# Performance work log

Measured on AMD Instinct MI355X. Metric: run time of the kernel, lower is better.

Reference implementation:

```python
import jax, jax.numpy as jnp
import numpy as np
from math import sqrt

B, N, M, HID, NH = 16, 512, 1024, 512, 8
HS = HID // NH  # 64


def layer_norm(x, g, b, eps=1e-5):
    mu = jnp.mean(x, axis=-1, keepdims=True)
    var = jnp.var(x, axis=-1, keepdims=True)
    return (x - mu) * jax.lax.rsqrt(var + eps) * g + b


def apply_moverz(x, s, c):
    # x: [B, L, NH, HS]; s, c: [B, L, 1, HS//2]
    x0, x1 = x[..., 0::2], x[..., 1::2]
    return jnp.concatenate([x0 * c - x1 * s, x1 * c + x0 * s], axis=-1)


def attention(q, k, v, mask):
    # q: [B,Nq,NH,HS], k/v: [B,Nk,NH,HS], mask broadcastable to [B,NH,Nq,Nk]
    attn = jnp.einsum('bnhd,bmhd->bhnm', q, k) / sqrt(HS)
    attn = jnp.where(mask, -jnp.inf, attn)
    attn = jax.nn.softmax(attn, axis=-1)
    x = jnp.einsum('bhnm,bmhd->bnhd', attn, v)
    return x.reshape(x.shape[0], x.shape[1], HID)


def setup_inputs() -> dict:
    key = jax.random.key(0)
    ks = jax.random.split(key, 24)
    inp = {}
    inp['tgt'] = jax.random.normal(ks[0], (B, N, HID), dtype=jnp.float32)
    inp['mem'] = jax.random.normal(ks[1], (B, M, HID), dtype=jnp.float32)
    th_p = jax.random.uniform(ks[2], (B, N, 1, HS // 2), dtype=jnp.float32) * (2 * np.pi)
    th_k = jax.random.uniform(ks[3], (B, M, 1, HS // 2), dtype=jnp.float32) * (2 * np.pi)
    inp['pep_mass_sin'] = jnp.sin(th_p)
    inp['pep_mass_cos'] = jnp.cos(th_p)
    inp['peaks_moverz_sin'] = jnp.sin(th_k)
    inp['peaks_moverz_cos'] = jnp.cos(th_k)
    # causal self-attn mask (True = masked)
    inp['tgt_mask'] = jnp.triu(jnp.ones((N, N), dtype=bool), k=1)[None, None]
    # pad last 64 memory positions
    pad = jnp.arange(M) >= (M - 64)
    inp['mem_key_padding_mask'] = jnp.broadcast_to(pad[None, None, None, :], (B, 1, 1, M))
    s = 0.02
    w = lambda i, shape: jax.random.normal(ks[i], shape, dtype=jnp.float32) * s
    # MaskedMultiHeadAttn params
    inp['mmha_w'] = w(4, (3 * HID, HID)); inp['mmha_b'] = jnp.zeros((3 * HID,), jnp.float32)
    inp['mmha_ow'] = w(5, (HID, HID)); inp['mmha_ob'] = jnp.zeros((HID,), jnp.float32)
    inp['mmha_g'] = jnp.ones((HID,), jnp.float32); inp['mmha_beta'] = jnp.zeros((HID,), jnp.float32)
    # MultiHeadAttn (cross) params
    inp['mha_qw'] = w(6, (HID, HID)); inp['mha_qb'] = jnp.zeros((HID,), jnp.float32)
    inp['mha_kvw'] = w(7, (2 * HID, HID)); inp['mha_kvb'] = jnp.zeros((2 * HID,), jnp.float32)
    inp['mha_ow'] = w(8, (HID, HID)); inp['mha_ob'] = jnp.zeros((HID,), jnp.float32)
    inp['mha_g'] = jnp.ones((HID,), jnp.float32); inp['mha_beta'] = jnp.zeros((HID,), jnp.float32)
    # FFN params (no bias)
    inp['ffn_w1'] = w(9, (4 * HID, HID))
    inp['ffn_w2'] = w(10, (HID, 4 * HID))
    inp['ffn_g'] = jnp.ones((HID,), jnp.float32); inp['ffn_beta'] = jnp.zeros((HID,), jnp.float32)
    return inp


def reference(tgt, mem, pep_mass_sin, pep_mass_cos, peaks_moverz_sin, peaks_moverz_cos,
              tgt_mask, mem_key_padding_mask,
              mmha_w, mmha_b, mmha_ow, mmha_ob, mmha_g, mmha_beta,
              mha_qw, mha_qb, mha_kvw, mha_kvb, mha_ow, mha_ob, mha_g, mha_beta,
              ffn_w1, ffn_w2, ffn_g, ffn_beta):
    # --- masked self-attention ---
    qkv = (tgt @ mmha_w.T + mmha_b).reshape(B, N, NH, 3 * HS)
    q, k, v = jnp.split(qkv, 3, axis=-1)
    x = attention(q, k, v, tgt_mask)
    tgt = layer_norm(x @ mmha_ow.T + mmha_ob + tgt, mmha_g, mmha_beta)
    # --- cross-attention with moverz distance bias ---
    q = (tgt @ mha_qw.T + mha_qb).reshape(B, N, NH, HS)
    q = apply_moverz(q, pep_mass_sin, pep_mass_cos)
    kv = (mem @ mha_kvw.T + mha_kvb).reshape(B, M, NH, 2 * HS)
    k, v = jnp.split(kv, 2, axis=-1)
    k = apply_moverz(k, peaks_moverz_sin, peaks_moverz_cos)
    x = attention(q, k, v, mem_key_padding_mask)
    tgt = layer_norm(x @ mha_ow.T + mha_ob + tgt, mha_g, mha_beta)
    # --- FFN ---
    h = jax.nn.relu(tgt @ ffn_w1.T) @ ffn_w2.T
    tgt = layer_norm(tgt + h, ffn_g, ffn_beta)
    return tgt
```

## Files before the change

kernel.cpp:

```cpp
#include <hip/hip_runtime.h>
#include <hip/hip_bf16.h>

#define BB 16
#define NN 512
#define MM 1024
#define HIDD 512
#define NHH 8

typedef unsigned short ushort_t;
typedef __attribute__((ext_vector_type(8))) short short8;
typedef __attribute__((ext_vector_type(8))) _Float16 half8;
typedef __attribute__((ext_vector_type(4))) _Float16 half4;
typedef __attribute__((ext_vector_type(4))) float f32x4;

__device__ __forceinline__ ushort_t f2bf(float x) {
    unsigned u = __float_as_uint(x);
    u += 0x7fff + ((u >> 16) & 1);
    return (ushort_t)(u >> 16);
}

#define GLD16(g, l) __builtin_amdgcn_global_load_lds(                      \
    (const __attribute__((address_space(1))) void*)(g),                    \
    (__attribute__((address_space(3))) void*)(l), 16, 0, 0)

__device__ __forceinline__ void xcd_swizzle(int& colb, int& rowb) {
    int id = blockIdx.x + blockIdx.y * gridDim.x;
    int C = gridDim.x;
    int xcd = id & 7;
    int slot = id >> 3;
    int rows_per = gridDim.y >> 3;
    colb = slot % C;
    rowb = xcd * rows_per + slot / C;
}

__global__ __launch_bounds__(256)
void gemm_bf(const ushort_t* __restrict__ A, const ushort_t* __restrict__ W,
             const float* __restrict__ bias, float* __restrict__ C,
             ushort_t* __restrict__ Cb, _Float16* __restrict__ Ch,
             int K, int Cout, int relu) {
    __shared__ ushort_t As[128 * 32];
    __shared__ ushort_t Ws[128 * 32];
    const int tid = threadIdx.x;
    const int lane = tid & 63;
    const int wid = tid >> 6;
    const int wm = wid >> 1, wn = wid & 1;
    int colb, rowb;
    xcd_swizzle(colb, rowb);
    const long row0 = (long)rowb * 128;
    const long col0 = (long)colb * 128;

    const int sr = lane >> 2;
    const int skq = lane & 3;
    const ushort_t* Ag = A + (row0 + wid * 32 + sr) * (long)K + skq * 8;
    const ushort_t* Wg = W + (col0 + wid * 32 + sr) * (long)K + skq * 8;
    ushort_t* As0 = &As[(wid * 32) * 32];
    ushort_t* As1 = &As[(wid * 32 + 16) * 32];
    ushort_t* Ws0 = &Ws[(wid * 32) * 32];
    ushort_t* Ws1 = &Ws[(wid * 32 + 16) * 32];

    f32x4 acc[4][4] = {};
    const int lr = lane & 15;
    const int kg = lane >> 4;

    for (int k0 = 0; k0 < K; k0 += 32) {
        __syncthreads();
        GLD16(Ag + k0, As0);
        GLD16(Ag + 16 * (long)K + k0, As1);
        GLD16(Wg + k0, Ws0);
        GLD16(Wg + 16 * (long)K + k0, Ws1);
        __syncthreads();
        short8 af[4], bfr[4];
#pragma unroll
        for (int i = 0; i < 4; i++)
            af[i] = *(const short8*)&As[(wm * 64 + i * 16 + lr) * 32 + kg * 8];
#pragma unroll
        for (int j = 0; j < 4; j++)
            bfr[j] = *(const short8*)&Ws[(wn * 64 + j * 16 + lr) * 32 + kg * 8];
#pragma unroll
        for (int i = 0; i < 4; i++)
#pragma unroll
            for (int j = 0; j < 4; j++)
                acc[i][j] = __builtin_amdgcn_mfma_f32_16x16x32_bf16(
                    af[i], bfr[j], acc[i][j], 0, 0, 0);
    }

#pragma unroll
    for (int i = 0; i < 4; i++) {
#pragma unroll
        for (int j = 0; j < 4; j++) {
            long row = row0 + wm * 64 + i * 16 + kg * 4;
            long col = col0 + wn * 64 + j * 16 + lr;
            float bv = bias ? bias[col] : 0.f;
#pragma unroll
            for (int r = 0; r < 4; r++) {
                float x = acc[i][j][r] + bv;
                if (relu) x = fmaxf(x, 0.f);
                size_t idx = (row + r) * (size_t)Cout + col;
                if (Ch)      Ch[idx] = (_Float16)x;
                else if (Cb) Cb[idx] = f2bf(x);
                else         C[idx] = x;
            }
        }
    }
}

__global__ __launch_bounds__(256)
void gemm_bf64(const ushort_t* __restrict__ A, const ushort_t* __restrict__ W,
               const float* __restrict__ bias, float* __restrict__ C,
               ushort_t* __restrict__ Cb, _Float16* __restrict__ Ch,
               int K, int Cout, int relu) {
    __shared__ ushort_t As[128 * 32];
    __shared__ ushort_t Ws[64 * 32];
    const int tid = threadIdx.x;
    const int lane = tid & 63;
    const int w = tid >> 6;
    int colb, rowb;
    xcd_swizzle(colb, rowb);
    const long row0 = (long)rowb * 128;
    const long col0 = (long)colb * 64;

    const int sr = lane >> 2;
    const int skq = lane & 3;
    const ushort_t* Ag = A + (row0 + w * 32 + sr) * (long)K + skq * 8;
    const ushort_t* Wg = W + (col0 + w * 16 + sr) * (long)K + skq * 8;
    ushort_t* As0 = &As[(w * 32) * 32];
    ushort_t* As1 = &As[(w * 32 + 16) * 32];
    ushort_t* Ws0 = &Ws[(w * 16) * 32];

    f32x4 acc[2][4] = {};
    const int lr = lane & 15;
    const int kg = lane >> 4;

    for (int k0 = 0; k0 < K; k0 += 32) {
        __syncthreads();
        GLD16(Ag + k0, As0);
        GLD16(Ag + 16 * (long)K + k0, As1);
        GLD16(Wg + k0, Ws0);
        __syncthreads();
        short8 af[2], bfr[4];
#pragma unroll
        for (int i = 0; i < 2; i++)
            af[i] = *(const short8*)&As[(w * 32 + i * 16 + lr) * 32 + kg * 8];
#pragma unroll
        for (int j = 0; j < 4; j++)
            bfr[j] = *(const short8*)&Ws[(j * 16 + lr) * 32 + kg * 8];
#pragma unroll
        for (int i = 0; i < 2; i++)
#pragma unroll
            for (int j = 0; j < 4; j++)
                acc[i][j] = __builtin_amdgcn_mfma_f32_16x16x32_bf16(
                    af[i], bfr[j], acc[i][j], 0, 0, 0);
    }

#pragma unroll
    for (int i = 0; i < 2; i++) {
#pragma unroll
        for (int j = 0; j < 4; j++) {
            long row = row0 + w * 32 + i * 16 + kg * 4;
            long col = col0 + j * 16 + lr;
            float bv = bias ? bias[col] : 0.f;
#pragma unroll
            for (int r = 0; r < 4; r++) {
                float x = acc[i][j][r] + bv;
                if (relu) x = fmaxf(x, 0.f);
                size_t idx = (row + r) * (size_t)Cout + col;
                if (Ch)      Ch[idx] = (_Float16)x;
                else if (Cb) Cb[idx] = f2bf(x);
                else         C[idx] = x;
            }
        }
    }
}

__global__ __launch_bounds__(256)
void gemm_q_rot(const ushort_t* __restrict__ A, const ushort_t* __restrict__ W,
                const float* __restrict__ bias,
                const float* __restrict__ sn, const float* __restrict__ cs,
                _Float16* __restrict__ Qrot) {
    __shared__ ushort_t As[128 * 32];
    __shared__ ushort_t Ws[64 * 32];
    __shared__ _Float16 Cs[128][76];
    const int K = 512;
    const int tid = threadIdx.x;
    const int lane = tid & 63;
    const int w = tid >> 6;
    int colb, rowb;
    xcd_swizzle(colb, rowb);
    const long row0 = (long)rowb * 128;
    const int h = colb;
    const long col0 = (long)h * 64;

    const int sr = lane >> 2;
    const int skq = lane & 3;
    const ushort_t* Ag = A + (row0 + w * 32 + sr) * (long)K + skq * 8;
    const ushort_t* Wg = W + (col0 + w * 16 + sr) * (long)K + skq * 8;
    ushort_t* As0 = &As[(w * 32) * 32];
    ushort_t* As1 = &As[(w * 32 + 16) * 32];
    ushort_t* Ws0 = &Ws[(w * 16) * 32];

    f32x4 acc[2][4] = {};
    const int lr = lane & 15;
    const int kg = lane >> 4;

    for (int k0 = 0; k0 < K; k0 += 32) {
        __syncthreads();
        GLD16(Ag + k0, As0);
        GLD16(Ag + 16 * (long)K + k0, As1);
        GLD16(Wg + k0, Ws0);
        __syncthreads();
        short8 af[2], bfr[4];
#pragma unroll
        for (int i = 0; i < 2; i++)
            af[i] = *(const short8*)&As[(w * 32 + i * 16 + lr) * 32 + kg * 8];
#pragma unroll
        for (int j = 0; j < 4; j++)
            bfr[j] = *(const short8*)&Ws[(j * 16 + lr) * 32 + kg * 8];
#pragma unroll
        for (int i = 0; i < 2; i++)
#pragma unroll
            for (int j = 0; j < 4; j++)
                acc[i][j] = __builtin_amdgcn_mfma_f32_16x16x32_bf16(
                    af[i], bfr[j], acc[i][j], 0, 0, 0);
    }

#pragma unroll
    for (int i = 0; i < 2; i++)
#pragma unroll
        for (int j = 0; j < 4; j++) {
            int row = w * 32 + i * 16 + kg * 4;
            int col = j * 16 + lr;
            float bv = bias[col0 + col];
#pragma unroll
            for (int r = 0; r < 4; r++)
                Cs[row + r][col] = (_Float16)(acc[i][j][r] + bv);
        }
    __syncthreads();
    for (int idx = tid; idx < 4096; idx += 256) {
        int rr = idx >> 5, j = idx & 31;
        size_t srow = (size_t)row0 + rr;
        float x0 = (float)Cs[rr][2 * j], x1 = (float)Cs[rr][2 * j + 1];
        float s = sn[srow * 32 + j], c = cs[srow * 32 + j];
        Qrot[srow * 512 + h * 64 + j]      = (_Float16)(x0 * c - x1 * s);
        Qrot[srow * 512 + h * 64 + 32 + j] = (_Float16)(x1 * c + x0 * s);
    }
}

__global__ __launch_bounds__(256)
void gemm_kv(const ushort_t* __restrict__ A, const ushort_t* __restrict__ W,
             const float* __restrict__ bias,
             const float* __restrict__ sn, const float* __restrict__ cs,
             _Float16* __restrict__ Krot, _Float16* __restrict__ Vth) {
    __shared__ ushort_t As[128 * 32];
    __shared__ ushort_t Ws[128 * 32];
    __shared__ _Float16 Cs[128][76];
    const int K = 512;
    const int tid = threadIdx.x;
    const int lane = tid & 63;
    const int wid = tid >> 6;
    const int wm = wid >> 1, wn = wid & 1;
    int colb, rowb;
    xcd_swizzle(colb, rowb);
    const long row0 = (long)rowb * 128;
    const int h = colb;
    const long col0 = (long)h * 128;

    const int sr = lane >> 2;
    const int skq = lane & 3;
    const ushort_t* Ag = A + (row0 + wid * 32 + sr) * (long)K + skq * 8;
    const ushort_t* Wg = W + (col0 + wid * 32 + sr) * (long)K + skq * 8;
    ushort_t* As0 = &As[(wid * 32) * 32];
    ushort_t* As1 = &As[(wid * 32 + 16) * 32];
    ushort_t* Ws0 = &Ws[(wid * 32) * 32];
    ushort_t* Ws1 = &Ws[(wid * 32 + 16) * 32];

    f32x4 acc[4][4] = {};
    const int lr = lane & 15;
    const int kg = lane >> 4;

    for (int k0 = 0; k0 < K; k0 += 32) {
        __syncthreads();
        GLD16(Ag + k0, As0);
        GLD16(Ag + 16 * (long)K + k0, As1);
        GLD16(Wg + k0, Ws0);
        GLD16(Wg + 16 * (long)K + k0, Ws1);
        __syncthreads();
        short8 af[4], bfr[4];
#pragma unroll
        for (int i = 0; i < 4; i++)
            af[i] = *(const short8*)&As[(wm * 64 + i * 16 + lr) * 32 + kg * 8];
#pragma unroll
        for (int j = 0; j < 4; j++)
            bfr[j] = *(const short8*)&Ws[(wn * 64 + j * 16 + lr) * 32 + kg * 8];
#pragma unroll
        for (int i = 0; i < 4; i++)
#pragma unroll
            for (int j = 0; j < 4; j++)
                acc[i][j] = __builtin_amdgcn_mfma_f32_16x16x32_bf16(
                    af[i], bfr[j], acc[i][j], 0, 0, 0);
    }

    const int b_ = (int)(row0 >> 10);
    const int m0_ = (int)(row0 & 1023);
#pragma unroll
    for (int half = 0; half < 2; half++) {
        __syncthreads();
        if (wn == half) {
#pragma unroll
            for (int i = 0; i < 4; i++)
#pragma unroll
                for (int j = 0; j < 4; j++) {
                    int row = wm * 64 + i * 16 + kg * 4;
                    int col = j * 16 + lr;
                    float bv = bias[col0 + half * 64 + col];
#pragma unroll
                    for (int r = 0; r < 4; r++)
                        Cs[row + r][col] = (_Float16)(acc[i][j][r] + bv);
                }
        }
        __syncthreads();
        if (half == 0) {
            for (int idx = tid; idx < 4096; idx += 256) {
                int rr = idx >> 5, j = idx & 31;
                size_t srow = (size_t)row0 + rr;
                float x0 = (float)Cs[rr][2 * j], x1 = (float)Cs[rr][2 * j + 1];
                float s = sn[srow * 32 + j], c = cs[srow * 32 + j];
                Krot[srow * 512 + h * 64 + j]      = (_Float16)(x0 * c - x1 * s);
                Krot[srow * 512 + h * 64 + 32 + j] = (_Float16)(x1 * c + x0 * s);
            }
        } else {
            for (int idx = tid; idx < 1024; idx += 256) {
                int d = idx >> 4, c = idx & 15;
                half8 v;
#pragma unroll
                for (int k = 0; k < 8; k++) v[k] = Cs[c * 8 + k][d];
                *(half8*)(Vth + (((size_t)(b_ * NHH + h)) * 64 + d) * MM
                          + m0_ + c * 8) = v;
            }
        }
    }
}

__global__ __launch_bounds__(256)
void cvt_all(const float* __restrict__ tgt, const float* __restrict__ mem,
             const float* __restrict__ w0, const float* __restrict__ w1,
             const float* __restrict__ w2, const float* __restrict__ w3,
             const float* __restrict__ w4, const float* __restrict__ w5,
             const float* __restrict__ w6,
             ushort_t* __restrict__ Abf, ushort_t* __restrict__ membf,
             ushort_t* __restrict__ Wbf) {
    int blk = blockIdx.x;
    const float* src;
    ushort_t* dst;
    size_t off;
    if (blk < 4096)       { src = tgt; dst = Abf;   off = (size_t)blk * 1024; }
    else if (blk < 12288) { src = mem; dst = membf; off = (size_t)(blk - 4096) * 1024; }
    else {
        int wb = blk - 12288;
        dst = Wbf + (size_t)wb * 1024;
        if (wb < 768)       { src = w0; off = (size_t)wb * 1024; }
        else if (wb < 1024) { src = w1; off = (size_t)(wb - 768) * 1024; }
        else if (wb < 1280) { src = w2; off = (size_t)(wb - 1024) * 1024; }
        else if (wb < 1792) { src = w3; off = (size_t)(wb - 1280) * 1024; }
        else if (wb < 2048) { src = w4; off = (size_t)(wb - 1792) * 1024; }
        else if (wb < 3072) { src = w5; off = (size_t)(wb - 2048) * 1024; }
        else                { src = w6; off = (size_t)(wb - 3072) * 1024; }
        float4 v = *(const float4*)(src + off + threadIdx.x * 4);
        ushort4 o;
        o.x = f2bf(v.x); o.y = f2bf(v.y); o.z = f2bf(v.z); o.w = f2bf(v.w);
        *(ushort4*)(dst + threadIdx.x * 4) = o;
        return;
    }
    float4 v = *(const float4*)(src + off + threadIdx.x * 4);
    ushort4 o;
    o.x = f2bf(v.x); o.y = f2bf(v.y); o.z = f2bf(v.z); o.w = f2bf(v.w);
    *(ushort4*)(dst + off + threadIdx.x * 4) = o;
}

__global__ __launch_bounds__(256)
void prep_vt(const _Float16* __restrict__ src, int L, int stride,
             int hmul, int hadd, _Float16* __restrict__ Vt) {
    const int b = blockIdx.z, h = blockIdx.y, m0 = blockIdx.x * 64;
    const int tid = threadIdx.x;
    __shared__ _Float16 vt[64][72];
    for (int idx = tid; idx < 512; idx += 256) {
        int m = idx >> 3, c = idx & 7;
        half8 v = *(const half8*)(src + ((size_t)(b * L + m0 + m)) * stride
                                  + h * hmul + hadd + c * 8);
#pragma unroll
        for (int k = 0; k < 8; k++) vt[c * 8 + k][m] = v[k];
    }
    __syncthreads();
    for (int idx = tid; idx < 512; idx += 256) {
        int d = idx >> 3, c = idx & 7;
        *(half8*)(Vt + (((size_t)(b * NHH + h)) * 64 + d) * L + m0 + c * 8)
            = *(const half8*)&vt[d][c * 8];
    }
}

__global__ __launch_bounds__(256)
void attn2(const _Float16* __restrict__ Q, int qstride, int qmul, int qadd,
           const _Float16* __restrict__ K, int kstride, int kmul, int kadd,
           const _Float16* __restrict__ Vt, int LV, int Lrows,
           ushort_t* __restrict__ out, int kvlen, int causal) {
    const int g = blockIdx.x;
    const int bh = (g & 7) * 16 + ((g >> 3) & 15);
    const int qb = g >> 7;
    const int b = bh >> 3, h = bh & 7;
    const int n0 = qb * 128;
    const int tid = threadIdx.x, lane = tid & 63, w = tid >> 6;
    const int quad = lane >> 4, l16 = lane & 15;
    const int qw = n0 + w * 32;

    __shared__ _Float16 Ks[64 * 72];
    __shared__ _Float16 Vs[64 * 72];
    __shared__ _Float16 Ps[4][32 * 72];
    _Float16* Pw = Ps[w];

    half8 bq[2][2];
#pragma unroll
    for (int s = 0; s < 2; s++)
#pragma unroll
        for (int c = 0; c < 2; c++)
            bq[s][c] = *(const half8*)(Q + ((size_t)(b * NN + qw + s * 16 + l16)) * qstride
                                       + h * qmul + qadd + c * 32 + quad * 8);

    f32x4 acc[2][4] = {};
    float mrun[2] = {-3e38f, -3e38f}, lrun[2] = {0.f, 0.f};

    const int srow = tid >> 3;
    const int scol = (tid & 7) * 8;
    const int limit = causal ? (n0 + 128) : kvlen;

    half8 kr0, kr1, vr0, vr1;
    {
        size_t kb = ((size_t)(b * Lrows + srow)) * kstride + h * kmul + kadd + scol;
        kr0 = *(const half8*)(K + kb);
        kr1 = *(const half8*)(K + kb + (size_t)32 * kstride);
        size_t vb = (((size_t)(b * NHH + h)) * 64 + srow) * (size_t)LV + scol;
        vr0 = *(const half8*)(Vt + vb);
        vr1 = *(const half8*)(Vt + vb + (size_t)32 * LV);
    }

    for (int key0 = 0; key0 < limit; key0 += 64) {
        __syncthreads();
        *(half8*)&Ks[srow * 72 + scol] = kr0;
        *(half8*)&Ks[(srow + 32) * 72 + scol] = kr1;
        *(half8*)&Vs[srow * 72 + scol] = vr0;
        *(half8*)&Vs[(srow + 32) * 72 + scol] = vr1;
        __syncthreads();
        int knext = key0 + 64;
        if (knext < limit) {
            size_t kb = ((size_t)(b * Lrows + knext + srow)) * kstride
                        + h * kmul + kadd + scol;
            kr0 = *(const half8*)(K + kb);
            kr1 = *(const half8*)(K + kb + (size_t)32 * kstride);
            size_t vb = (((size_t)(b * NHH + h)) * 64 + srow) * (size_t)LV
                        + knext + scol;
            vr0 = *(const half8*)(Vt + vb);
            vr1 = *(const half8*)(Vt + vb + (size_t)32 * LV);
        }
        if (causal && key0 > qw + 31) continue;

        f32x4 st[2][4];
#pragma unroll
        for (int kt = 0; kt < 4; kt++) {
            half8 ak0 = *(const half8*)&Ks[(kt * 16 + l16) * 72 + quad * 8];
            half8 ak1 = *(const half8*)&Ks[(kt * 16 + l16) * 72 + 32 + quad * 8];
#pragma unroll
            for (int s = 0; s < 2; s++) {
                f32x4 z = {};
                z = __builtin_amdgcn_mfma_f32_16x16x32_f16(ak0, bq[s][0], z, 0, 0, 0);
                z = __builtin_amdgcn_mfma_f32_16x16x32_f16(ak1, bq[s][1], z, 0, 0, 0);
                st[s][kt] = z;
            }
        }
        if (causal && key0 + 64 > qw) {
#pragma unroll
            for (int s = 0; s < 2; s++) {
                int qabs = qw + s * 16 + l16;
#pragma unroll
                for (int kt = 0; kt < 4; kt++)
#pragma unroll
                    for (int r = 0; r < 4; r++)
                        if (key0 + kt * 16 + quad * 4 + r > qabs)
                            st[s][kt][r] = -3e38f;
            }
        }
#pragma unroll
        for (int s = 0; s < 2; s++) {
            float lm = -3e38f;
#pragma unroll
            for (int kt = 0; kt < 4; kt++)
                lm = fmaxf(lm, fmaxf(fmaxf(st[s][kt][0], st[s][kt][1]),
                                     fmaxf(st[s][kt][2], st[s][kt][3])));
            lm = fmaxf(lm, __shfl_xor(lm, 16));
            lm = fmaxf(lm, __shfl_xor(lm, 32));
            float mnew = fmaxf(mrun[s], lm);
            float corr = __expf((mrun[s] - mnew) * 0.125f);
            mrun[s] = mnew;
            float ls = 0.f;
#pragma unroll
            for (int kt = 0; kt < 4; kt++) {
                half4 ph;
#pragma unroll
                for (int r = 0; r < 4; r++) {
                    float p = __expf((st[s][kt][r] - mnew) * 0.125f);
                    ls += p;
                    ph[r] = (_Float16)p;
                }
                *(half4*)&Pw[(s * 16 + l16) * 72 + kt * 16 + quad * 4] = ph;
            }
            ls += __shfl_xor(ls, 16);
            ls += __shfl_xor(ls, 32);
            lrun[s] = lrun[s] * corr + ls;
            float cb0 = __shfl(corr, (lane & 48) | (quad * 4 + 0));
            float cb1 = __shfl(corr, (lane & 48) | (quad * 4 + 1));
            float cb2 = __shfl(corr, (lane & 48) | (quad * 4 + 2));
            float cb3 = __shfl(corr, (lane & 48) | (quad * 4 + 3));
#pragma unroll
            for (int dt = 0; dt < 4; dt++) {
                acc[s][dt][0] *= cb0; acc[s][dt][1] *= cb1;
                acc[s][dt][2] *= cb2; acc[s][dt][3] *= cb3;
            }
        }
        half8 ap[2][2];
#pragma unroll
        for (int s = 0; s < 2; s++)
#pragma unroll
            for (int c = 0; c < 2; c++)
                ap[s][c] = *(const half8*)&Pw[(s * 16 + l16) * 72 + c * 32 + quad * 8];
#pragma unroll
        for (int dt = 0; dt < 4; dt++) {
            half8 bv0 = *(const half8*)&Vs[(dt * 16 + l16) * 72 + quad * 8];
            half8 bv1 = *(const half8*)&Vs[(dt * 16 + l16) * 72 + 32 + quad * 8];
#pragma unroll
            for (int s = 0; s < 2; s++) {
                acc[s][dt] = __builtin_amdgcn_mfma_f32_16x16x32_f16(ap[s][0], bv0, acc[s][dt], 0, 0, 0);
                acc[s][dt] = __builtin_amdgcn_mfma_f32_16x16x32_f16(ap[s][1], bv1, acc[s][dt], 0, 0, 0);
            }
        }
    }
#pragma unroll
    for (int s = 0; s < 2; s++) {
        float invq = 1.f / lrun[s];
        float iv0 = __shfl(invq, (lane & 48) | (quad * 4 + 0));
        float iv1 = __shfl(invq, (lane & 48) | (quad * 4 + 1));
        float iv2 = __shfl(invq, (lane & 48) | (quad * 4 + 2));
        float iv3 = __shfl(invq, (lane & 48) | (quad * 4 + 3));
#pragma unroll
        for (int dt = 0; dt < 4; dt++) {
            size_t base = ((size_t)(b * NN + qw + s * 16 + quad * 4)) * 512
                          + h * 64 + dt * 16 + l16;
            out[base]           = f2bf(acc[s][dt][0] * iv0);
            out[base + 512]     = f2bf(acc[s][dt][1] * iv1);
            out[base + 1024]    = f2bf(acc[s][dt][2] * iv2);
            out[base + 1536]    = f2bf(acc[s][dt][3] * iv3);
        }
    }
}

__global__ __launch_bounds__(256)
void ln_residual(const float* __restrict__ u, int nsplit,
                 const float* __restrict__ res,
                 const float* __restrict__ g, const float* __restrict__ be,
                 float* __restrict__ out, ushort_t* __restrict__ outbf) {
    const int row = blockIdx.x, t = threadIdx.x;
    const float* rp = res + (size_t)row * HIDD;
    float z0 = rp[t];
    float z1 = rp[t + 256];
    for (int s = 0; s < nsplit; s++) {
        const float* up = u + (size_t)s * 4194304 + (size_t)row * HIDD;
        z0 += up[t];
        z1 += up[t + 256];
    }
    float sm = z0 + z1, s2 = z0 * z0 + z1 * z1;
#pragma unroll
    for (int off = 1; off < 64; off <<= 1) {
        sm += __shfl_xor(sm, off, 64);
        s2 += __shfl_xor(s2, off, 64);
    }
    __shared__ float ps[4], ps2[4];
    int w = t >> 6;
    if ((t & 63) == 0) { ps[w] = sm; ps2[w] = s2; }
    __syncthreads();
    sm = ps[0] + ps[1] + ps[2] + ps[3];
    s2 = ps2[0] + ps2[1] + ps2[2] + ps2[3];
    float mu = sm * (1.f / 512.f);
    float var = s2 * (1.f / 512.f) - mu * mu;
    float rstd = rsqrtf(var + 1e-5f);
    float y0 = (z0 - mu) * rstd * g[t] + be[t];
    float y1 = (z1 - mu) * rstd * g[t + 256] + be[t + 256];
    out[(size_t)row * HIDD + t]       = y0;
    out[(size_t)row * HIDD + t + 256] = y1;
    if (outbf) {
        outbf[(size_t)row * HIDD + t]       = f2bf(y0);
        outbf[(size_t)row * HIDD + t + 256] = f2bf(y1);
    }
}

extern "C" void kernel_launch(void* const* d_in, const int* in_sizes, int n_in,
                              void* d_out, int out_size, void* d_ws, size_t ws_size,
                              hipStream_t stream) {
    const float* tgt      = (const float*)d_in[0];
    const float* mem      = (const float*)d_in[1];
    const float* pep_sin  = (const float*)d_in[2];
    const float* pep_cos  = (const float*)d_in[3];
    const float* pk_sin   = (const float*)d_in[4];
    const float* pk_cos   = (const float*)d_in[5];
    const float* mmha_w   = (const float*)d_in[8];
    const float* mmha_b   = (const float*)d_in[9];
    const float* mmha_ow  = (const float*)d_in[10];
    const float* mmha_ob  = (const float*)d_in[11];
    const float* mmha_g   = (const float*)d_in[12];
    const float* mmha_be  = (const float*)d_in[13];
    const float* mha_qw   = (const float*)d_in[14];
    const float* mha_qb   = (const float*)d_in[15];
    const float* mha_kvw  = (const float*)d_in[16];
    const float* mha_kvb  = (const float*)d_in[17];
    const float* mha_ow   = (const float*)d_in[18];
    const float* mha_ob   = (const float*)d_in[19];
    const float* mha_g    = (const float*)d_in[20];
    const float* mha_be   = (const float*)d_in[21];
    const float* ffn_w1   = (const float*)d_in[22];
    const float* ffn_w2   = (const float*)d_in[23];
    const float* ffn_g    = (const float*)d_in[24];
    const float* ffn_be   = (const float*)d_in[25];

    float* ws = (float*)d_ws;
    float* utmp  = ws;
    float* tgt12 = ws + 4194304;
    _Float16* hp = (_Float16*)(ws + 8388608);
    _Float16* qkvh  = hp;
    _Float16* Qrot  = hp + 12582912;
    _Float16* Vth   = hp + 16777216;
    _Float16* Krot  = hp + 25165824;
    ushort_t* membf = (ushort_t*)(hp + 33554432);
    ushort_t* Abf   = (ushort_t*)(hp + 41943040);
    ushort_t* Wbf   = (ushort_t*)(hp + 46137344);
    ushort_t* w_mmha = Wbf;
    ushort_t* w_mmow = Wbf + 786432;
    ushort_t* w_qw   = Wbf + 1048576;
    ushort_t* w_kvw  = Wbf + 1310720;
    ushort_t* w_mow  = Wbf + 1835008;
    ushort_t* w_f1   = Wbf + 2097152;
    ushort_t* w_f2   = Wbf + 3145728;
    ushort_t* hbf = (ushort_t*)qkvh;
    float* out = (float*)d_out;
    (void)in_sizes; (void)n_in; (void)out_size; (void)ws_size;

    cvt_all<<<16384, 256, 0, stream>>>(tgt, mem, mmha_w, mmha_ow, mha_qw,
                                       mha_kvw, mha_ow, ffn_w1, ffn_w2,
                                       Abf, membf, Wbf);
    gemm_bf<<<dim3(12, 64), 256, 0, stream>>>(Abf, w_mmha, mmha_b, nullptr, nullptr, qkvh, 512, 1536, 0);
    prep_vt<<<dim3(8, NHH, BB), 256, 0, stream>>>(qkvh, NN, 1536, 192, 128, Vth);
    attn2<<<512, 256, 0, stream>>>(qkvh, 1536, 192, 0, qkvh, 1536, 192, 64,
                                   Vth, NN, NN, Abf, 0, 1);
    gemm_bf64<<<dim3(8, 64), 256, 0, stream>>>(Abf, w_mmow, mmha_ob, utmp, nullptr, nullptr, 512, 512, 0);
    ln_residual<<<8192, 256, 0, stream>>>(utmp, 1, tgt, mmha_g, mmha_be, tgt12, Abf);
    gemm_q_rot<<<dim3(8, 64), 256, 0, stream>>>(Abf, w_qw, mha_qb, pep_sin, pep_cos, Qrot);
    gemm_kv<<<dim3(8, 128), 256, 0, stream>>>(membf, w_kvw, mha_kvb, pk_sin, pk_cos, Krot, Vth);
    attn2<<<512, 256, 0, stream>>>(Qrot, 512, 64, 0, Krot, 512, 64, 0,
                                   Vth, MM, MM, Abf, MM - 64, 0);
    gemm_bf64<<<dim3(8, 64), 256, 0, stream>>>(Abf, w_mow, mha_ob, utmp, nullptr, nullptr, 512, 512, 0);
    ln_residual<<<8192, 256, 0, stream>>>(utmp, 1, tgt12, mha_g, mha_be, tgt12, Abf);
    gemm_bf<<<dim3(16, 64), 256, 0, stream>>>(Abf, w_f1, nullptr, nullptr, hbf, nullptr, 512, 2048, 1);
    gemm_bf64<<<dim3(8, 64), 256, 0, stream>>>(hbf, w_f2, nullptr, utmp, nullptr, nullptr, 2048, 512, 0);
    ln_residual<<<8192, 256, 0, stream>>>(utmp, 1, tgt12, ffn_g, ffn_be, out, nullptr);
}
```

Baseline: 430.6 us.

## Double-buffer LDS tiles in GEMM kernels to overlap loads with MFMA

All four bf16 GEMM kernels now use two LDS stages. The loads for the next K-slice are issued asynchronously into the other buffer while MFMAs run on the current one, which cuts the per-iteration barriers from two to one. The aim is to hide global-to-LDS latency behind compute. In the rotation and KV epilogue kernels, the fp16 staging tile now aliases the double-buffer storage, and an extra barrier guards that reuse. Correctness depends on the barrier also waiting for the outstanding async loads to finish.

```diff
diff --git a/kernel.cpp b/kernel.cpp
--- a/kernel.cpp
+++ b/kernel.cpp
@@ -38,8 +38,7 @@
              const float* __restrict__ bias, float* __restrict__ C,
              ushort_t* __restrict__ Cb, _Float16* __restrict__ Ch,
              int K, int Cout, int relu) {
-    __shared__ ushort_t As[128 * 32];
-    __shared__ ushort_t Ws[128 * 32];
+    __shared__ __align__(16) ushort_t smem[2][8192];
     const int tid = threadIdx.x;
     const int lane = tid & 63;
     const int wid = tid >> 6;
@@ -53,29 +52,36 @@
     const int skq = lane & 3;
     const ushort_t* Ag = A + (row0 + wid * 32 + sr) * (long)K + skq * 8;
     const ushort_t* Wg = W + (col0 + wid * 32 + sr) * (long)K + skq * 8;
-    ushort_t* As0 = &As[(wid * 32) * 32];
-    ushort_t* As1 = &As[(wid * 32 + 16) * 32];
-    ushort_t* Ws0 = &Ws[(wid * 32) * 32];
-    ushort_t* Ws1 = &Ws[(wid * 32 + 16) * 32];
+    const int sa0 = (wid * 32) * 32, sa1 = (wid * 32 + 16) * 32;
 
     f32x4 acc[4][4] = {};
     const int lr = lane & 15;
     const int kg = lane >> 4;
 
-    for (int k0 = 0; k0 < K; k0 += 32) {
-        __syncthreads();
-        GLD16(Ag + k0, As0);
-        GLD16(Ag + 16 * (long)K + k0, As1);
-        GLD16(Wg + k0, Ws0);
-        GLD16(Wg + 16 * (long)K + k0, Ws1);
-        __syncthreads();
+    GLD16(Ag, &smem[0][sa0]);
+    GLD16(Ag + 16 * (long)K, &smem[0][sa1]);
+    GLD16(Wg, &smem[0][4096 + sa0]);
+    GLD16(Wg + 16 * (long)K, &smem[0][4096 + sa1]);
+
+    int pb = 0;
+    for (int k0 = 0; k0 < K; k0 += 32, pb ^= 1) {
+        __syncthreads();
+        int kn = k0 + 32;
+        if (kn < K) {
+            GLD16(Ag + kn, &smem[pb ^ 1][sa0]);
+            GLD16(Ag + 16 * (long)K + kn, &smem[pb ^ 1][sa1]);
+            GLD16(Wg + kn, &smem[pb ^ 1][4096 + sa0]);
+            GLD16(Wg + 16 * (long)K + kn, &smem[pb ^ 1][4096 + sa1]);
+        }
+        const ushort_t* Ab = smem[pb];
+        const ushort_t* Wb = smem[pb] + 4096;
         short8 af[4], bfr[4];
 #pragma unroll
         for (int i = 0; i < 4; i++)
-            af[i] = *(const short8*)&As[(wm * 64 + i * 16 + lr) * 32 + kg * 8];
+            af[i] = *(const short8*)&Ab[(wm * 64 + i * 16 + lr) * 32 + kg * 8];
 #pragma unroll
         for (int j = 0; j < 4; j++)
-            bfr[j] = *(const short8*)&Ws[(wn * 64 + j * 16 + lr) * 32 + kg * 8];
+            bfr[j] = *(const short8*)&Wb[(wn * 64 + j * 16 + lr) * 32 + kg * 8];
 #pragma unroll
         for (int i = 0; i < 4; i++)
 #pragma unroll
@@ -109,8 +115,7 @@
                const float* __restrict__ bias, float* __restrict__ C,
                ushort_t* __restrict__ Cb, _Float16* __restrict__ Ch,
                int K, int Cout, int relu) {
-    __shared__ ushort_t As[128 * 32];
-    __shared__ ushort_t Ws[64 * 32];
+    __shared__ __align__(16) ushort_t smem[2][6144];
     const int tid = threadIdx.x;
     const int lane = tid & 63;
     const int w = tid >> 6;
@@ -123,27 +128,35 @@
     const int skq = lane & 3;
     const ushort_t* Ag = A + (row0 + w * 32 + sr) * (long)K + skq * 8;
     const ushort_t* Wg = W + (col0 + w * 16 + sr) * (long)K + skq * 8;
-    ushort_t* As0 = &As[(w * 32) * 32];
-    ushort_t* As1 = &As[(w * 32 + 16) * 32];
-    ushort_t* Ws0 = &Ws[(w * 16) * 32];
+    const int sa0 = (w * 32) * 32, sa1 = (w * 32 + 16) * 32;
+    const int sw0 = 4096 + (w * 16) * 32;
 
     f32x4 acc[2][4] = {};
     const int lr = lane & 15;
     const int kg = lane >> 4;
 
-    for (int k0 = 0; k0 < K; k0 += 32) {
-        __syncthreads();
-        GLD16(Ag + k0, As0);
-        GLD16(Ag + 16 * (long)K + k0, As1);
-        GLD16(Wg + k0, Ws0);
-        __syncthreads();
+    GLD16(Ag, &smem[0][sa0]);
+    GLD16(Ag + 16 * (long)K, &smem[0][sa1]);
+    GLD16(Wg, &smem[0][sw0]);
+
+    int pb = 0;
+    for (int k0 = 0; k0 < K; k0 += 32, pb ^= 1) {
+        __syncthreads();
+        int kn = k0 + 32;
+        if (kn < K) {
+            GLD16(Ag + kn, &smem[pb ^ 1][sa0]);
+            GLD16(Ag + 16 * (long)K + kn, &smem[pb ^ 1][sa1]);
+            GLD16(Wg + kn, &smem[pb ^ 1][sw0]);
+        }
+        const ushort_t* Ab = smem[pb];
+        const ushort_t* Wb = smem[pb] + 4096;
         short8 af[2], bfr[4];
 #pragma unroll
         for (int i = 0; i < 2; i++)
-            af[i] = *(const short8*)&As[(w * 32 + i * 16 + lr) * 32 + kg * 8];
+            af[i] = *(const short8*)&Ab[(w * 32 + i * 16 + lr) * 32 + kg * 8];
 #pragma unroll
         for (int j = 0; j < 4; j++)
-            bfr[j] = *(const short8*)&Ws[(j * 16 + lr) * 32 + kg * 8];
+            bfr[j] = *(const short8*)&Wb[(j * 16 + lr) * 32 + kg * 8];
 #pragma unroll
         for (int i = 0; i < 2; i++)
 #pragma unroll
@@ -177,9 +190,8 @@
                 const float* __restrict__ bias,
                 const float* __restrict__ sn, const float* __restrict__ cs,
                 _Float16* __restrict__ Qrot) {
-    __shared__ ushort_t As[128 * 32];
-    __shared__ ushort_t Ws[64 * 32];
-    __shared__ _Float16 Cs[128][76];
+    __shared__ __align__(16) ushort_t smem[2][6144];
+    _Float16* Cs = (_Float16*)smem;
     const int K = 512;
     const int tid = threadIdx.x;
     const int lane = tid & 63;
@@ -194,27 +206,35 @@
     const int skq = lane & 3;
     const ushort_t* Ag = A + (row0 + w * 32 + sr) * (long)K + skq * 8;
     const ushort_t* Wg = W + (col0 + w * 16 + sr) * (long)K + skq * 8;
-    ushort_t* As0 = &As[(w * 32) * 32];
-    ushort_t* As1 = &As[(w * 32 + 16) * 32];
-    ushort_t* Ws0 = &Ws[(w * 16) * 32];
+    const int sa0 = (w * 32) * 32, sa1 = (w * 32 + 16) * 32;
+    const int sw0 = 4096 + (w * 16) * 32;
 
     f32x4 acc[2][4] = {};
     const int lr = lane & 15;
     const int kg = lane >> 4;
 
-    for (int k0 = 0; k0 < K; k0 += 32) {
-        __syncthreads();
-        GLD16(Ag + k0, As0);
-        GLD16(Ag + 16 * (long)K + k0, As1);
-        GLD16(Wg + k0, Ws0);
-        __syncthreads();
+    GLD16(Ag, &smem[0][sa0]);
+    GLD16(Ag + 16 * (long)K, &smem[0][sa1]);
+    GLD16(Wg, &smem[0][sw0]);
+
+    int pb = 0;
+    for (int k0 = 0; k0 < K; k0 += 32, pb ^= 1) {
+        __syncthreads();
+        int kn = k0 + 32;
+        if (kn < K) {
+            GLD16(Ag + kn, &smem[pb ^ 1][sa0]);
+            GLD16(Ag + 16 * (long)K + kn, &smem[pb ^ 1][sa1]);
+            GLD16(Wg + kn, &smem[pb ^ 1][sw0]);
+        }
+        const ushort_t* Ab = smem[pb];
+        const ushort_t* Wb = smem[pb] + 4096;
         short8 af[2], bfr[4];
 #pragma unroll
         for (int i = 0; i < 2; i++)
-            af[i] = *(const short8*)&As[(w * 32 + i * 16 + lr) * 32 + kg * 8];
+            af[i] = *(const short8*)&Ab[(w * 32 + i * 16 + lr) * 32 + kg * 8];
 #pragma unroll
         for (int j = 0; j < 4; j++)
-            bfr[j] = *(const short8*)&Ws[(j * 16 + lr) * 32 + kg * 8];
+            bfr[j] = *(const short8*)&Wb[(j * 16 + lr) * 32 + kg * 8];
 #pragma unroll
         for (int i = 0; i < 2; i++)
 #pragma unroll
@@ -223,6 +243,7 @@
                     af[i], bfr[j], acc[i][j], 0, 0, 0);
     }
 
+    __syncthreads();
 #pragma unroll
     for (int i = 0; i < 2; i++)
 #pragma unroll
@@ -232,13 +253,13 @@
             float bv = bias[col0 + col];
 #pragma unroll
             for (int r = 0; r < 4; r++)
-                Cs[row + r][col] = (_Float16)(acc[i][j][r] + bv);
+                Cs[(row + r) * 76 + col] = (_Float16)(acc[i][j][r] + bv);
         }
     __syncthreads();
     for (int idx = tid; idx < 4096; idx += 256) {
         int rr = idx >> 5, j = idx & 31;
         size_t srow = (size_t)row0 + rr;
-        float x0 = (float)Cs[rr][2 * j], x1 = (float)Cs[rr][2 * j + 1];
+        float x0 = (float)Cs[rr * 76 + 2 * j], x1 = (float)Cs[rr * 76 + 2 * j + 1];
         float s = sn[srow * 32 + j], c = cs[srow * 32 + j];
         Qrot[srow * 512 + h * 64 + j]      = (_Float16)(x0 * c - x1 * s);
         Qrot[srow * 512 + h * 64 + 32 + j] = (_Float16)(x1 * c + x0 * s);
@@ -250,9 +271,8 @@
              const float* __restrict__ bias,
              const float* __restrict__ sn, const float* __restrict__ cs,
              _Float16* __restrict__ Krot, _Float16* __restrict__ Vth) {
-    __shared__ ushort_t As[128 * 32];
-    __shared__ ushort_t Ws[128 * 32];
-    __shared__ _Float16 Cs[128][76];
+    __shared__ __align__(16) ushort_t smem[2][8192];
+    _Float16* Cs = (_Float16*)smem;
     const int K = 512;
     const int tid = threadIdx.x;
     const int lane = tid & 63;
@@ -268,29 +288,36 @@
     const int skq = lane & 3;
     const ushort_t* Ag = A + (row0 + wid * 32 + sr) * (long)K + skq * 8;
     const ushort_t* Wg = W + (col0 + wid * 32 + sr) * (long)K + skq * 8;
-    ushort_t* As0 = &As[(wid * 32) * 32];
-    ushort_t* As1 = &As[(wid * 32 + 16) * 32];
-    ushort_t* Ws0 = &Ws[(wid * 32) * 32];
-    ushort_t* Ws1 = &Ws[(wid * 32 + 16) * 32];
+    const int sa0 = (wid * 32) * 32, sa1 = (wid * 32 + 16) * 32;
 
     f32x4 acc[4][4] = {};
     const int lr = lane & 15;
     const int kg = lane >> 4;
 
-    for (int k0 = 0; k0 < K; k0 += 32) {
-        __syncthreads();
-        GLD16(Ag + k0, As0);
-        GLD16(Ag + 16 * (long)K + k0, As1);
-        GLD16(Wg + k0, Ws0);
-        GLD16(Wg + 16 * (long)K + k0, Ws1);
-        __syncthreads();
+    GLD16(Ag, &smem[0][sa0]);
+    GLD16(Ag + 16 * (long)K, &smem[0][sa1]);
+    GLD16(Wg, &smem[0][4096 + sa0]);
+    GLD16(Wg + 16 * (long)K, &smem[0][4096 + sa1]);
+
+    int pb = 0;
+    for (int k0 = 0; k0 < K; k0 += 32, pb ^= 1) {
+        __syncthreads();
+        int kn = k0 + 32;
+        if (kn < K) {
+            GLD16(Ag + kn, &smem[pb ^ 1][sa0]);
+            GLD16(Ag + 16 * (long)K + kn, &smem[pb ^ 1][sa1]);
+            GLD16(Wg + kn, &smem[pb ^ 1][4096 + sa0]);
+            GLD16(Wg + 16 * (long)K + kn, &smem[pb ^ 1][4096 + sa1]);
+        }
+        const ushort_t* Ab = smem[pb];
+        const ushort_t* Wb = smem[pb] + 4096;
         short8 af[4], bfr[4];
 #pragma unroll
         for (int i = 0; i < 4; i++)
-            af[i] = *(const short8*)&As[(wm * 64 + i * 16 + lr) * 32 + kg * 8];
+            af[i] = *(const short8*)&Ab[(wm * 64 + i * 16 + lr) * 32 + kg * 8];
 #pragma unroll
         for (int j = 0; j < 4; j++)
-            bfr[j] = *(const short8*)&Ws[(wn * 64 + j * 16 + lr) * 32 + kg * 8];
+            bfr[j] = *(const short8*)&Wb[(wn * 64 + j * 16 + lr) * 32 + kg * 8];
 #pragma unroll
         for (int i = 0; i < 4; i++)
 #pragma unroll
@@ -314,7 +341,7 @@
                     float bv = bias[col0 + half * 64 + col];
 #pragma unroll
                     for (int r = 0; r < 4; r++)
-                        Cs[row + r][col] = (_Float16)(acc[i][j][r] + bv);
+                        Cs[(row + r) * 76 + col] = (_Float16)(acc[i][j][r] + bv);
                 }
         }
         __syncthreads();
@@ -322,7 +349,7 @@
             for (int idx = tid; idx < 4096; idx += 256) {
                 int rr = idx >> 5, j = idx & 31;
                 size_t srow = (size_t)row0 + rr;
-                float x0 = (float)Cs[rr][2 * j], x1 = (float)Cs[rr][2 * j + 1];
+                float x0 = (float)Cs[rr * 76 + 2 * j], x1 = (float)Cs[rr * 76 + 2 * j + 1];
                 float s = sn[srow * 32 + j], c = cs[srow * 32 + j];
                 Krot[srow * 512 + h * 64 + j]      = (_Float16)(x0 * c - x1 * s);
                 Krot[srow * 512 + h * 64 + 32 + j] = (_Float16)(x1 * c + x0 * s);
@@ -332,7 +359,7 @@
                 int d = idx >> 4, c = idx & 15;
                 half8 v;
 #pragma unroll
-                for (int k = 0; k < 8; k++) v[k] = Cs[c * 8 + k][d];
+                for (int k = 0; k < 8; k++) v[k] = Cs[(c * 8 + k) * 76 + d];
                 *(half8*)(Vth + (((size_t)(b_ * NHH + h)) * 64 + d) * MM
                           + m0_ + c * 8) = v;
             }
```

Result: faster. 414.5 us (-3.8%).
